# Kernel optimization log

Hardware: AMD Instinct MI355X
Metric: run time of the kernel (lower is better)

Reference implementation:

```python
import jax, jax.numpy as jnp
import numpy as np

B, L, D, H = 2, 2048, 1024, 16
DH = D // H  # 64

def setup_inputs() -> dict:
    key = jax.random.key(0)
    ks = jax.random.split(key, 5)
    s = 1.0 / np.sqrt(D)
    return {
        "x": jax.random.normal(ks[0], (B, L, D), jnp.float32),
        "Wk": jax.random.normal(ks[1], (D, D), jnp.float32) * s,
        "Wq": jax.random.normal(ks[2], (D, D), jnp.float32) * s,
        "Wv": jax.random.normal(ks[3], (D, D), jnp.float32) * s,
        "Wo": jax.random.normal(ks[4], (D, D), jnp.float32) * s,
    }

def reference(x, Wk, Wq, Wv, Wo):
    # Linear(D,D,bias=False): y = x @ W.T ; W stored [out,in] as in torch
    k = (x @ Wk.T).reshape(B, L, H, DH).transpose(0, 2, 1, 3)  # [B,H,L,dh]
    q = (x @ Wq.T).reshape(B, L, H, DH).transpose(0, 2, 1, 3)
    v = (x @ Wv.T).reshape(B, L, H, DH).transpose(0, 2, 1, 3)
    att = jnp.einsum("bhqd,bhkd->bhqk", q, k) / jnp.sqrt(jnp.float32(DH))
    causal = jnp.tril(jnp.ones((L, L), dtype=bool))
    att = jnp.where(causal, att, -jnp.inf)
    p = jax.nn.softmax(att, axis=-1)  # dropout omitted (eval mode)
    out = jnp.einsum("bhqk,bhkd->bhqd", p, v)  # [B,H,L,dh]
    out = out.transpose(0, 2, 1, 3).reshape(B, L, D)
    return out @ Wo.T
```

## Files before the change

kernel.cpp:

```cpp
#include <hip/hip_runtime.h>

typedef __bf16 bf16_t;
typedef __bf16 bf16x8 __attribute__((ext_vector_type(8)));
typedef __bf16 bf16x4 __attribute__((ext_vector_type(4)));
typedef float f32x4 __attribute__((ext_vector_type(4)));

#define MFMA_BF16(a, b, c) __builtin_amdgcn_mfma_f32_16x16x32_bf16((a), (b), (c), 0, 0, 0)
#define LOG2E 1.44269504088896f

__device__ __forceinline__ void gload16(const bf16_t* g, bf16_t* l) {
  __builtin_amdgcn_global_load_lds(
      (__attribute__((address_space(1))) void*)(g),
      (__attribute__((address_space(3))) void*)(l), 16, 0, 0);
}

__global__ void cast_all(const float* __restrict__ x, const float* __restrict__ wk,
                         const float* __restrict__ wq, const float* __restrict__ wv,
                         const float* __restrict__ wo, bf16_t* __restrict__ xbf,
                         bf16_t* __restrict__ wbf) {
  const size_t NX = 4194304, NW = 1048576;
  size_t i = (size_t)blockIdx.x * blockDim.x + threadIdx.x;
  const size_t total4 = (NX + 4 * NW) / 4;
  const size_t stride = (size_t)gridDim.x * blockDim.x;
  for (; i < total4; i += stride) {
    size_t f = i * 4;
    const float* src;
    bf16_t* dst;
    if (f < NX) {
      src = x + f;
      dst = xbf + f;
    } else {
      size_t g = f - NX;
      size_t wsel = g >> 20;
      size_t off = g & (NW - 1);
      dst = wbf + g;
      src = (wsel == 0) ? wq + off : (wsel == 1) ? wk + off : (wsel == 2) ? wv + off : wo + off;
    }
    float4 v = *(const float4*)src;
    bf16x4 o;
    o[0] = (bf16_t)v.x; o[1] = (bf16_t)v.y; o[2] = (bf16_t)v.z; o[3] = (bf16_t)v.w;
    *(bf16x4*)dst = o;
  }
}

template <int BM, int BN, typename TOUT>
__global__ __launch_bounds__(256) void gemm_nt(const bf16_t* __restrict__ A,
                                               const bf16_t* __restrict__ W,
                                               TOUT* __restrict__ C, int K, int ldc,
                                               int blocksPerSect, bf16_t* __restrict__ vtb) {
  constexpr int MF = BM / 32;
  constexpr int NF = BN / 32;
  constexpr int ABYTES = BM * 128;
  constexpr int BBYTES = BN * 128;
  __shared__ bf16_t As[2][BM * 64];
  __shared__ bf16_t Bs[2][BN * 64];
  const int t = threadIdx.x;
  const int l = t & 63, w = t >> 6;
  const int wm = w >> 1;
  const int wn = w & 1;
  const int lr = l & 15, lg = l >> 4;
  const int bm = blockIdx.x;
  const int by = blockIdx.y;
  const int sect = by / blocksPerSect;
  const int bn = by - sect * blocksPerSect;
  const bf16_t* Wp = W + ((size_t)sect << 20);
  const int n0 = sect * 1024 + bn * BN;

  const int srow0 = t >> 3;
  const int csw = (t & 7) ^ (srow0 & 7);
  const bf16_t* ag = A + (size_t)(bm * BM + srow0) * K + csw * 8;
  const bf16_t* bg = Wp + (size_t)(bn * BN + srow0) * K + csw * 8;
  char* As0 = (char*)&As[0][0];
  char* Bs0 = (char*)&Bs[0][0];
  const int stg = t * 16;

#define GSTAGE(k0, sb)                                                                             \
  do {                                                                                             \
    _Pragma("unroll") for (int p = 0; p < BM / 32; ++p)                                            \
        gload16(ag + (size_t)(32 * p) * K + (k0), (bf16_t*)(As0 + (sb) * ABYTES + p * 4096 + stg)); \
    _Pragma("unroll") for (int p = 0; p < BN / 32; ++p)                                            \
        gload16(bg + (size_t)(32 * p) * K + (k0), (bf16_t*)(Bs0 + (sb) * BBYTES + p * 4096 + stg)); \
  } while (0)

  const int r7 = lr & 7;
  const int o0 = lr * 128 + ((lg ^ r7) * 16);
  const int abase = wm * (MF * 2048) + o0;
  const int bbase = wn * (NF * 2048) + o0;

  f32x4 acc[MF][NF];
#pragma unroll
  for (int i = 0; i < MF; ++i)
#pragma unroll
    for (int j = 0; j < NF; ++j) acc[i][j] = (f32x4){0.f, 0.f, 0.f, 0.f};

  GSTAGE(0, 0);
  __syncthreads();

  int cb = 0;
  for (int k0 = 0; k0 < K; k0 += 64) {
    if (k0 + 64 < K) GSTAGE(k0 + 64, cb ^ 1);
#pragma unroll
    for (int kk = 0; kk < 2; ++kk) {
      bf16x8 af[MF], bfr[NF];
#pragma unroll
      for (int mf = 0; mf < MF; ++mf)
        af[mf] = *(const bf16x8*)(As0 + cb * ABYTES + ((abase + mf * 2048) ^ (kk * 64)));
#pragma unroll
      for (int nf = 0; nf < NF; ++nf)
        bfr[nf] = *(const bf16x8*)(Bs0 + cb * BBYTES + ((bbase + nf * 2048) ^ (kk * 64)));
#pragma unroll
      for (int mf = 0; mf < MF; ++mf)
#pragma unroll
        for (int nf = 0; nf < NF; ++nf)
          acc[mf][nf] = MFMA_BF16(af[mf], bfr[nf], acc[mf][nf]);
    }
    __syncthreads();
    cb ^= 1;
  }
#undef GSTAGE

  if (vtb != nullptr && sect == 2) {
#pragma unroll
    for (int mf = 0; mf < MF; ++mf)
#pragma unroll
      for (int nf = 0; nf < NF; ++nf) {
        int row0 = bm * BM + wm * (MF * 16) + mf * 16 + lg * 4;
        int colg = bn * BN + wn * (NF * 16) + nf * 16 + lr;
        int bb = row0 >> 11, ll = row0 & 2047;
        size_t vaddr = ((size_t)((bb * 16 + (colg >> 6)) * 64 + (colg & 63))) * 2048 + ll;
        bf16x4 pk;
#pragma unroll
        for (int j = 0; j < 4; ++j) pk[j] = (bf16_t)acc[mf][nf][j];
        *(bf16x4*)(vtb + vaddr) = pk;
      }
    return;
  }
#pragma unroll
  for (int mf = 0; mf < MF; ++mf)
#pragma unroll
    for (int nf = 0; nf < NF; ++nf)
#pragma unroll
      for (int j = 0; j < 4; ++j) {
        int row = bm * BM + wm * (MF * 16) + mf * 16 + lg * 4 + j;
        int col = n0 + wn * (NF * 16) + nf * 16 + lr;
        C[(size_t)row * ldc + col] = (TOUT)acc[mf][nf][j];
      }
}

__global__ __launch_bounds__(256, 4) void attn_fwd(const bf16_t* __restrict__ qk,
                                                   const bf16_t* __restrict__ vt,
                                                   bf16_t* __restrict__ out) {
  __shared__ bf16_t Ks[2][4096];
  __shared__ bf16_t Vts[2][4096];
  __shared__ bf16_t Pt[4][1024];
  const int t = threadIdx.x, l = t & 63, w = t >> 6;
  const int lr = l & 15, lg = l >> 4;
  const int n = blockIdx.x;
  const int bh = n & 31;
  const int b = bh >> 4, h = bh & 15;
  const int m = n >> 5;
  const int j8 = m & 7, kk = m >> 3;
  const int qt = (kk == 0) ? j8 : (kk == 1) ? 15 - j8 : (kk == 2) ? 16 + j8 : 31 - j8;
  const int qloc = w * 16 + lr;
  const int qrow = qt * 64 + qloc;

  const float SCINIT = -12.f * LOG2E;

  const int srow = t >> 3, sc8 = t & 7;
  const int cs = sc8 ^ (srow & 7);
  const bf16_t* kbase = qk + ((size_t)(b * 2048 + srow)) * 2048 + 1024 + h * 64 + cs * 8;
  const bf16_t* vbase = vt + ((size_t)(bh * 64 + srow)) * 2048 + cs * 8;
  char* Ks0 = (char*)&Ks[0][0];
  char* Vt0 = (char*)&Vts[0][0];
  const int stg = t * 16;

#define STAGE(ktile, sboff)                                                   \
  do {                                                                        \
    const bf16_t* ks_ = kbase + (size_t)(ktile) * (64 * 2048);                \
    const bf16_t* vs_ = vbase + (size_t)(ktile) * 64;                         \
    gload16(ks_, (bf16_t*)(Ks0 + (sboff) + stg));                             \
    gload16(ks_ + (size_t)32 * 2048, (bf16_t*)(Ks0 + (sboff) + 4096 + stg));  \
    gload16(vs_, (bf16_t*)(Vt0 + (sboff) + stg));                             \
    gload16(vs_ + (size_t)32 * 2048, (bf16_t*)(Vt0 + (sboff) + 4096 + stg));  \
  } while (0)

  const float qsc = 0.125f * LOG2E;
  const bf16_t* Qg = qk + (size_t)(b * 2048 + qrow) * 2048 + h * 64 + lg * 8;
  bf16x8 qf0 = *(const bf16x8*)(Qg);
  bf16x8 qf1 = *(const bf16x8*)(Qg + 32);
#pragma unroll
  for (int jj = 0; jj < 8; ++jj) {
    qf0[jj] = (bf16_t)((float)qf0[jj] * qsc);
    qf1[jj] = (bf16_t)((float)qf1[jj] * qsc);
  }

  f32x4 acc[4];
#pragma unroll
  for (int df = 0; df < 4; ++df) acc[df] = (f32x4){0.f, 0.f, 0.f, 0.f};
  float l_r = 0.f;

  const int r7 = lr & 7;
  const int o0 = lr * 128 + ((lg ^ r7) * 16);
  const int o1 = lr * 128 + (((lg ^ 4) ^ r7) * 16);

  char* PwB = (char*)&Pt[w][0];
  const int psw = r7 << 4;
  int pwo[4];
#pragma unroll
  for (int nf = 0; nf < 4; ++nf) pwo[nf] = lr * 128 + ((nf * 32 + lg * 8) ^ psw);
  const int pr0 = lr * 128 + ((lg * 16) ^ psw);
  const int pr1 = lr * 128 + ((64 + lg * 16) ^ psw);

  STAGE(0, 0);
  __syncthreads();

  int boff = 0;
  for (int kt = 0; kt <= qt; ++kt) {
    if (kt < qt) STAGE(kt + 1, boff ^ 8192);

    f32x4 sc[4];
#pragma unroll
    for (int nf = 0; nf < 4; ++nf)
      sc[nf] = (f32x4){SCINIT, SCINIT, SCINIT, SCINIT};
    __builtin_amdgcn_s_setprio(1);
#pragma unroll
    for (int nf = 0; nf < 4; ++nf) {
      bf16x8 kf0 = *(const bf16x8*)(Ks0 + boff + nf * 2048 + o0);
      bf16x8 kf1 = *(const bf16x8*)(Ks0 + boff + nf * 2048 + o1);
      sc[nf] = MFMA_BF16(kf0, qf0, sc[nf]);
      sc[nf] = MFMA_BF16(kf1, qf1, sc[nf]);
    }
    __builtin_amdgcn_s_setprio(0);

    float p[16], ps = 0.f;
    if (kt == qt) {
#pragma unroll
      for (int nf = 0; nf < 4; ++nf)
#pragma unroll
        for (int jj = 0; jj < 4; ++jj) {
          float sv = sc[nf][jj];
          if (nf * 16 + lg * 4 + jj > qloc) sv = -1e30f;
          float pv = __builtin_amdgcn_exp2f(sv);
          p[nf * 4 + jj] = pv;
          ps += pv;
        }
    } else {
#pragma unroll
      for (int nf = 0; nf < 4; ++nf)
#pragma unroll
        for (int jj = 0; jj < 4; ++jj) {
          float pv = __builtin_amdgcn_exp2f(sc[nf][jj]);
          p[nf * 4 + jj] = pv;
          ps += pv;
        }
    }
    l_r += ps;

#pragma unroll
    for (int nf = 0; nf < 4; ++nf) {
      bf16x4 pk;
#pragma unroll
      for (int jj = 0; jj < 4; ++jj) pk[jj] = (bf16_t)p[nf * 4 + jj];
      *(bf16x4*)(PwB + pwo[nf]) = pk;
    }

    bf16x8 pb0 = *(const bf16x8*)(PwB + pr0);
    bf16x8 pb1 = *(const bf16x8*)(PwB + pr1);
    __builtin_amdgcn_s_setprio(1);
#pragma unroll
    for (int df = 0; df < 4; ++df) {
      bf16x8 vf0 = *(const bf16x8*)(Vt0 + boff + df * 2048 + o0);
      bf16x8 vf1 = *(const bf16x8*)(Vt0 + boff + df * 2048 + o1);
      acc[df] = MFMA_BF16(vf0, pb0, acc[df]);
      acc[df] = MFMA_BF16(vf1, pb1, acc[df]);
    }
    __builtin_amdgcn_s_setprio(0);
    __syncthreads();
    boff ^= 8192;
  }
#undef STAGE

  l_r += __shfl_xor(l_r, 16);
  l_r += __shfl_xor(l_r, 32);
  float inv = 1.f / l_r;
#pragma unroll
  for (int df = 0; df < 4; ++df) {
    bf16x4 o;
#pragma unroll
    for (int jj = 0; jj < 4; ++jj) o[jj] = (bf16_t)(acc[df][jj] * inv);
    *(bf16x4*)(out + (size_t)(b * 2048 + qrow) * 1024 + h * 64 + df * 16 + lg * 4) = o;
  }
}

extern "C" void kernel_launch(void* const* d_in, const int* in_sizes, int n_in,
                              void* d_out, int out_size, void* d_ws, size_t ws_size,
                              hipStream_t stream) {
  const float* x = (const float*)d_in[0];
  const float* wk = (const float*)d_in[1];
  const float* wq = (const float*)d_in[2];
  const float* wv = (const float*)d_in[3];
  const float* wo = (const float*)d_in[4];

  bf16_t* xbf = (bf16_t*)d_ws;
  bf16_t* wbf = xbf + 4194304;
  bf16_t* qkbf = wbf + 4194304;
  bf16_t* vtbuf = qkbf + 8388608;
  bf16_t* attnbf = xbf;
  float* out = (float*)d_out;

  cast_all<<<dim3(2048), dim3(256), 0, stream>>>(x, wk, wq, wv, wo, xbf, wbf);
  gemm_nt<128, 64, bf16_t><<<dim3(32, 48), dim3(256), 0, stream>>>(xbf, wbf, qkbf, 1024, 2048, 16,
                                                                   vtbuf);
  attn_fwd<<<dim3(1024), dim3(256), 0, stream>>>(qkbf, vtbuf, attnbf);
  gemm_nt<64, 64, float><<<dim3(64, 16), dim3(256), 0, stream>>>(attnbf, wbf + 3 * 1048576, out,
                                                                 1024, 1024, 16, (bf16_t*)nullptr);
}
```

Before: 98.49 us.

## Process two query tiles per attention block to reuse staged K/V tiles

Each attention workgroup now handles two adjacent 64-row query tiles, so every K/V tile staged into LDS feeds both sets of MFMAs. The grid is halved, and a new pairing scheme balances the causal work across blocks. The aim is to halve K/V global-to-LDS traffic and barrier overhead per query row. In exchange, register use per thread roughly doubles and launch bounds drop to 2 blocks per CU. Tile A also does one wasted, fully masked iteration at the diagonal of tile B.

```diff
diff --git a/kernel.cpp b/kernel.cpp
--- a/kernel.cpp
+++ b/kernel.cpp
@@ -147,22 +147,23 @@
       }
 }
 
-__global__ __launch_bounds__(256, 4) void attn_fwd(const bf16_t* __restrict__ qk,
+__global__ __launch_bounds__(256, 2) void attn_fwd(const bf16_t* __restrict__ qk,
                                                    const bf16_t* __restrict__ vt,
                                                    bf16_t* __restrict__ out) {
   __shared__ bf16_t Ks[2][4096];
   __shared__ bf16_t Vts[2][4096];
-  __shared__ bf16_t Pt[4][1024];
+  __shared__ bf16_t Pt[4][2048];
   const int t = threadIdx.x, l = t & 63, w = t >> 6;
   const int lr = l & 15, lg = l >> 4;
   const int n = blockIdx.x;
   const int bh = n & 31;
   const int b = bh >> 4, h = bh & 15;
   const int m = n >> 5;
-  const int j8 = m & 7, kk = m >> 3;
-  const int qt = (kk == 0) ? j8 : (kk == 1) ? 15 - j8 : (kk == 2) ? 16 + j8 : 31 - j8;
+  const int tq = (m < 8) ? m : 23 - m;
+  const int qtA = 2 * tq, qtB = 2 * tq + 1;
   const int qloc = w * 16 + lr;
-  const int qrow = qt * 64 + qloc;
+  const int qrowA = qtA * 64 + qloc;
+  const int qrowB = qrowA + 64;
 
   const float SCINIT = -12.f * LOG2E;
 
@@ -185,25 +186,34 @@
   } while (0)
 
   const float qsc = 0.125f * LOG2E;
-  const bf16_t* Qg = qk + (size_t)(b * 2048 + qrow) * 2048 + h * 64 + lg * 8;
-  bf16x8 qf0 = *(const bf16x8*)(Qg);
-  bf16x8 qf1 = *(const bf16x8*)(Qg + 32);
+  const bf16_t* QgA = qk + (size_t)(b * 2048 + qrowA) * 2048 + h * 64 + lg * 8;
+  const bf16_t* QgB = QgA + (size_t)64 * 2048;
+  bf16x8 qa0 = *(const bf16x8*)(QgA);
+  bf16x8 qa1 = *(const bf16x8*)(QgA + 32);
+  bf16x8 qb0 = *(const bf16x8*)(QgB);
+  bf16x8 qb1 = *(const bf16x8*)(QgB + 32);
 #pragma unroll
   for (int jj = 0; jj < 8; ++jj) {
-    qf0[jj] = (bf16_t)((float)qf0[jj] * qsc);
-    qf1[jj] = (bf16_t)((float)qf1[jj] * qsc);
-  }
-
-  f32x4 acc[4];
-#pragma unroll
-  for (int df = 0; df < 4; ++df) acc[df] = (f32x4){0.f, 0.f, 0.f, 0.f};
-  float l_r = 0.f;
+    qa0[jj] = (bf16_t)((float)qa0[jj] * qsc);
+    qa1[jj] = (bf16_t)((float)qa1[jj] * qsc);
+    qb0[jj] = (bf16_t)((float)qb0[jj] * qsc);
+    qb1[jj] = (bf16_t)((float)qb1[jj] * qsc);
+  }
+
+  f32x4 accA[4], accB[4];
+#pragma unroll
+  for (int df = 0; df < 4; ++df) {
+    accA[df] = (f32x4){0.f, 0.f, 0.f, 0.f};
+    accB[df] = (f32x4){0.f, 0.f, 0.f, 0.f};
+  }
+  float lA = 0.f, lB = 0.f;
 
   const int r7 = lr & 7;
   const int o0 = lr * 128 + ((lg ^ r7) * 16);
   const int o1 = lr * 128 + (((lg ^ 4) ^ r7) * 16);
 
-  char* PwB = (char*)&Pt[w][0];
+  char* PwA = (char*)&Pt[w][0];
+  char* PwBp = PwA + 2048;
   const int psw = r7 << 4;
   int pwo[4];
 #pragma unroll
@@ -215,64 +225,101 @@
   __syncthreads();
 
   int boff = 0;
-  for (int kt = 0; kt <= qt; ++kt) {
-    if (kt < qt) STAGE(kt + 1, boff ^ 8192);
-
-    f32x4 sc[4];
-#pragma unroll
-    for (int nf = 0; nf < 4; ++nf)
-      sc[nf] = (f32x4){SCINIT, SCINIT, SCINIT, SCINIT};
+  for (int kt = 0; kt <= qtB; ++kt) {
+    if (kt < qtB) STAGE(kt + 1, boff ^ 8192);
+
+    f32x4 scA[4], scB[4];
+#pragma unroll
+    for (int nf = 0; nf < 4; ++nf) {
+      scA[nf] = (f32x4){SCINIT, SCINIT, SCINIT, SCINIT};
+      scB[nf] = (f32x4){SCINIT, SCINIT, SCINIT, SCINIT};
+    }
     __builtin_amdgcn_s_setprio(1);
 #pragma unroll
     for (int nf = 0; nf < 4; ++nf) {
       bf16x8 kf0 = *(const bf16x8*)(Ks0 + boff + nf * 2048 + o0);
       bf16x8 kf1 = *(const bf16x8*)(Ks0 + boff + nf * 2048 + o1);
-      sc[nf] = MFMA_BF16(kf0, qf0, sc[nf]);
-      sc[nf] = MFMA_BF16(kf1, qf1, sc[nf]);
+      scB[nf] = MFMA_BF16(kf0, qb0, scB[nf]);
+      scB[nf] = MFMA_BF16(kf1, qb1, scB[nf]);
+      scA[nf] = MFMA_BF16(kf0, qa0, scA[nf]);
+      scA[nf] = MFMA_BF16(kf1, qa1, scA[nf]);
     }
     __builtin_amdgcn_s_setprio(0);
 
-    float p[16], ps = 0.f;
-    if (kt == qt) {
+    float pA[16], psA = 0.f;
+    if (kt >= qtA) {
+      const bool allm = (kt > qtA);
 #pragma unroll
       for (int nf = 0; nf < 4; ++nf)
 #pragma unroll
         for (int jj = 0; jj < 4; ++jj) {
-          float sv = sc[nf][jj];
+          float sv = scA[nf][jj];
+          if (allm || nf * 16 + lg * 4 + jj > qloc) sv = -1e30f;
+          float pv = __builtin_amdgcn_exp2f(sv);
+          pA[nf * 4 + jj] = pv;
+          psA += pv;
+        }
+    } else {
+#pragma unroll
+      for (int nf = 0; nf < 4; ++nf)
+#pragma unroll
+        for (int jj = 0; jj < 4; ++jj) {
+          float pv = __builtin_amdgcn_exp2f(scA[nf][jj]);
+          pA[nf * 4 + jj] = pv;
+          psA += pv;
+        }
+    }
+    lA += psA;
+
+    float pB[16], psB = 0.f;
+    if (kt == qtB) {
+#pragma unroll
+      for (int nf = 0; nf < 4; ++nf)
+#pragma unroll
+        for (int jj = 0; jj < 4; ++jj) {
+          float sv = scB[nf][jj];
           if (nf * 16 + lg * 4 + jj > qloc) sv = -1e30f;
           float pv = __builtin_amdgcn_exp2f(sv);
-          p[nf * 4 + jj] = pv;
-          ps += pv;
+          pB[nf * 4 + jj] = pv;
+          psB += pv;
         }
     } else {
 #pragma unroll
       for (int nf = 0; nf < 4; ++nf)
 #pragma unroll
         for (int jj = 0; jj < 4; ++jj) {
-          float pv = __builtin_amdgcn_exp2f(sc[nf][jj]);
-          p[nf * 4 + jj] = pv;
-          ps += pv;
+          float pv = __builtin_amdgcn_exp2f(scB[nf][jj]);
+          pB[nf * 4 + jj] = pv;
+          psB += pv;
         }
     }
-    l_r += ps;
+    lB += psB;
 
 #pragma unroll
     for (int nf = 0; nf < 4; ++nf) {
-      bf16x4 pk;
-#pragma unroll
-      for (int jj = 0; jj < 4; ++jj) pk[jj] = (bf16_t)p[nf * 4 + jj];
-      *(bf16x4*)(PwB + pwo[nf]) = pk;
-    }
-
-    bf16x8 pb0 = *(const bf16x8*)(PwB + pr0);
-    bf16x8 pb1 = *(const bf16x8*)(PwB + pr1);
+      bf16x4 ka, kb;
+#pragma unroll
+      for (int jj = 0; jj < 4; ++jj) {
+        ka[jj] = (bf16_t)pA[nf * 4 + jj];
+        kb[jj] = (bf16_t)pB[nf * 4 + jj];
+      }
+      *(bf16x4*)(PwA + pwo[nf]) = ka;
+      *(bf16x4*)(PwBp + pwo[nf]) = kb;
+    }
+
+    bf16x8 pa0 = *(const bf16x8*)(PwA + pr0);
+    bf16x8 pa1 = *(const bf16x8*)(PwA + pr1);
+    bf16x8 pb0 = *(const bf16x8*)(PwBp + pr0);
+    bf16x8 pb1 = *(const bf16x8*)(PwBp + pr1);
     __builtin_amdgcn_s_setprio(1);
 #pragma unroll
     for (int df = 0; df < 4; ++df) {
       bf16x8 vf0 = *(const bf16x8*)(Vt0 + boff + df * 2048 + o0);
       bf16x8 vf1 = *(const bf16x8*)(Vt0 + boff + df * 2048 + o1);
-      acc[df] = MFMA_BF16(vf0, pb0, acc[df]);
-      acc[df] = MFMA_BF16(vf1, pb1, acc[df]);
+      accB[df] = MFMA_BF16(vf0, pb0, accB[df]);
+      accB[df] = MFMA_BF16(vf1, pb1, accB[df]);
+      accA[df] = MFMA_BF16(vf0, pa0, accA[df]);
+      accA[df] = MFMA_BF16(vf1, pa1, accA[df]);
     }
     __builtin_amdgcn_s_setprio(0);
     __syncthreads();
@@ -280,15 +327,21 @@
   }
 #undef STAGE
 
-  l_r += __shfl_xor(l_r, 16);
-  l_r += __shfl_xor(l_r, 32);
-  float inv = 1.f / l_r;
+  lA += __shfl_xor(lA, 16);
+  lA += __shfl_xor(lA, 32);
+  lB += __shfl_xor(lB, 16);
+  lB += __shfl_xor(lB, 32);
+  float invA = 1.f / lA, invB = 1.f / lB;
 #pragma unroll
   for (int df = 0; df < 4; ++df) {
-    bf16x4 o;
-#pragma unroll
-    for (int jj = 0; jj < 4; ++jj) o[jj] = (bf16_t)(acc[df][jj] * inv);
-    *(bf16x4*)(out + (size_t)(b * 2048 + qrow) * 1024 + h * 64 + df * 16 + lg * 4) = o;
+    bf16x4 oa, ob;
+#pragma unroll
+    for (int jj = 0; jj < 4; ++jj) {
+      oa[jj] = (bf16_t)(accA[df][jj] * invA);
+      ob[jj] = (bf16_t)(accB[df][jj] * invB);
+    }
+    *(bf16x4*)(out + (size_t)(b * 2048 + qrowA) * 1024 + h * 64 + df * 16 + lg * 4) = oa;
+    *(bf16x4*)(out + (size_t)(b * 2048 + qrowB) * 1024 + h * 64 + df * 16 + lg * 4) = ob;
   }
 }
 
@@ -311,7 +364,7 @@
   cast_all<<<dim3(2048), dim3(256), 0, stream>>>(x, wk, wq, wv, wo, xbf, wbf);
   gemm_nt<128, 64, bf16_t><<<dim3(32, 48), dim3(256), 0, stream>>>(xbf, wbf, qkbf, 1024, 2048, 16,
                                                                    vtbuf);
-  attn_fwd<<<dim3(1024), dim3(256), 0, stream>>>(qkbf, vtbuf, attnbf);
+  attn_fwd<<<dim3(512), dim3(256), 0, stream>>>(qkbf, vtbuf, attnbf);
   gemm_nt<64, 64, float><<<dim3(64, 16), dim3(256), 0, stream>>>(attnbf, wbf + 3 * 1048576, out,
                                                                  1024, 1024, 16, (bf16_t*)nullptr);
 }
```

Result: slower. 104.8 us (+6.4%).
